# Optimization experiments

Hardware: AMD Instinct MI355X
Metric: run time of the kernel (lower is better)

The kernel has to match this reference:

```python
import jax, jax.numpy as jnp
import numpy as np

N_NODES = 100000
N_EDGES = 1250000
N_FEAT = 64
HIDDEN = 16
N_CLASSES = 7


def setup_inputs() -> dict:
    key = jax.random.key(0)
    ks = jax.random.split(key, 10)
    x = jax.random.normal(ks[0], (N_NODES, N_FEAT), dtype=jnp.float32)
    edge_index = jax.random.randint(ks[1], (2, N_EDGES), 0, N_NODES, dtype=jnp.int64)
    s = 0.1
    return {
        "x": x,
        "edge_index": edge_index,
        # conv1 MLP: Linear(F,16) ReLU Linear(16,16) ReLU
        "W1": jax.random.normal(ks[2], (N_FEAT, HIDDEN), dtype=jnp.float32) * s,
        "b1": jnp.zeros((HIDDEN,), dtype=jnp.float32),
        "W2": jax.random.normal(ks[3], (HIDDEN, HIDDEN), dtype=jnp.float32) * s,
        "b2": jnp.zeros((HIDDEN,), dtype=jnp.float32),
        # conv2 MLP: Linear(16,16) ReLU Linear(16,C)
        "W3": jax.random.normal(ks[4], (HIDDEN, HIDDEN), dtype=jnp.float32) * s,
        "b3": jnp.zeros((HIDDEN,), dtype=jnp.float32),
        "W4": jax.random.normal(ks[5], (HIDDEN, N_CLASSES), dtype=jnp.float32) * s,
        "b4": jnp.zeros((N_CLASSES,), dtype=jnp.float32),
    }


def _gin_aggregate(h, src, dst):
    # GINConv with default eps=0: (1+eps)*x + sum_{j in N(i)} x_j
    msgs = h[src]  # [E, d] gather
    agg = jax.ops.segment_sum(msgs, dst, num_segments=h.shape[0])  # scatter-add
    return h + agg


def reference(x, edge_index, W1, b1, W2, b2, W3, b3, W4, b4):
    src = edge_index[0]
    dst = edge_index[1]
    # conv1: GIN aggregate + MLP(Linear,ReLU,Linear,ReLU)
    h = _gin_aggregate(x, src, dst)
    h = jax.nn.relu(h @ W1 + b1)
    h = jax.nn.relu(h @ W2 + b2)
    # F.relu after conv1 (idempotent here, kept for faithfulness)
    h = jax.nn.relu(h)
    # conv2: GIN aggregate + MLP(Linear,ReLU,Linear)
    h = _gin_aggregate(h, src, dst)
    h = jax.nn.relu(h @ W3 + b3)
    h = h @ W4 + b4
    return jax.nn.log_softmax(h, axis=1)
```

## Files before the change

kernel.cpp:

```cpp
#include <hip/hip_runtime.h>
#include <math.h>

constexpr int NN = 100000;
constexpr int NE = 1250000;
constexpr int NF = 64;
constexpr int NH = 16;
constexpr int NC = 7;

constexpr int BKT_SHIFT = 7;
constexpr int BKT_NODES = 1 << BKT_SHIFT;
constexpr int NBUCKET = (NN + BKT_NODES - 1) / BKT_NODES;
constexpr int BSTRIDE = 2048;
constexpr int EPB = 8192;
constexpr int NBLK_BUCKET = (NE + EPB - 1) / EPB;
constexpr int CUR_PAD = 16;

__global__ __launch_bounds__(256) void k1_gemm(
    const float* __restrict__ x, const float* __restrict__ W1,
    const float* __restrict__ b1, float* __restrict__ A, float* __restrict__ B,
    int* __restrict__ gcur) {
    int gtid = blockIdx.x * 256 + threadIdx.x;
    if (gtid < NBUCKET * CUR_PAD) gcur[gtid] = 0;

    __shared__ float w[NF * NH];
    __shared__ float bias[NH];
    for (int i = threadIdx.x; i < NF * NH; i += blockDim.x) w[i] = W1[i];
    if (threadIdx.x < NH) bias[threadIdx.x] = b1[threadIdx.x];
    __syncthreads();
    int node = gtid;
    if (node >= NN) return;

    float acc[NH];
#pragma unroll
    for (int j = 0; j < NH; ++j) acc[j] = 0.f;

    const float4* xr = (const float4*)(x + (size_t)node * NF);
#pragma unroll
    for (int k4 = 0; k4 < NF / 4; ++k4) {
        float4 xv = xr[k4];
        int k = k4 * 4;
#pragma unroll
        for (int j = 0; j < NH; ++j) {
            acc[j] += xv.x * w[(k + 0) * NH + j]
                    + xv.y * w[(k + 1) * NH + j]
                    + xv.z * w[(k + 2) * NH + j]
                    + xv.w * w[(k + 3) * NH + j];
        }
    }
    float4* Ar = (float4*)(A + (size_t)node * NH);
    float4* Br = (float4*)(B + (size_t)node * NH);
#pragma unroll
    for (int q = 0; q < NH / 4; ++q) {
        float4 a;
        a.x = acc[q * 4 + 0]; a.y = acc[q * 4 + 1];
        a.z = acc[q * 4 + 2]; a.w = acc[q * 4 + 3];
        Ar[q] = a;
        float4 bv;
        bv.x = a.x + bias[q * 4 + 0]; bv.y = a.y + bias[q * 4 + 1];
        bv.z = a.z + bias[q * 4 + 2]; bv.w = a.w + bias[q * 4 + 3];
        Br[q] = bv;
    }
}

__global__ __launch_bounds__(1024) void k_bucket(
    const int* __restrict__ src, const int* __restrict__ dst,
    int* __restrict__ gcur, unsigned* __restrict__ gbuf) {
    __shared__ int cnt[NBUCKET];
    __shared__ int loff[NBUCKET];
    __shared__ int gb[NBUCKET];
    __shared__ int s[1024];
    __shared__ unsigned sorted[EPB];

    int tid = threadIdx.x;
    for (int i = tid; i < NBUCKET; i += 1024) cnt[i] = 0;
    __syncthreads();

    unsigned pk[8];
    int bk[8];
    int rk[8];
    int base = blockIdx.x * EPB;
    int nval = NE - base; if (nval > EPB) nval = EPB;
#pragma unroll
    for (int k = 0; k < 8; ++k) {
        int e = base + k * 1024 + tid;
        bk[k] = -1;
        if (e < NE) {
            int sv = src[e];
            int d = dst[e];
            int b = d >> BKT_SHIFT;
            bk[k] = b;
            pk[k] = ((unsigned)sv << BKT_SHIFT) | (unsigned)(d & (BKT_NODES - 1));
            rk[k] = atomicAdd(&cnt[b], 1);
        }
    }
    __syncthreads();

    int v = (tid < NBUCKET) ? cnt[tid] : 0;
    s[tid] = v;
    __syncthreads();
    for (int d = 1; d < 1024; d <<= 1) {
        int u = (tid >= d) ? s[tid - d] : 0;
        __syncthreads();
        s[tid] += u;
        __syncthreads();
    }
    if (tid < NBUCKET) {
        loff[tid] = s[tid] - v;
        gb[tid] = (v > 0) ? atomicAdd(&gcur[tid * CUR_PAD], v) : 0;
    }
    __syncthreads();

#pragma unroll
    for (int k = 0; k < 8; ++k) {
        if (bk[k] >= 0) sorted[loff[bk[k]] + rk[k]] = pk[k];
    }
    __syncthreads();

    for (int i = tid; i < nval; i += 1024) {
        int lo = 0, hi = NBUCKET - 1;
        while (lo < hi) {
            int mid = (lo + hi + 1) >> 1;
            if (loff[mid] <= i) lo = mid; else hi = mid - 1;
        }
        int pos = gb[lo] + (i - loff[lo]);
        if (pos < BSTRIDE)
            gbuf[(size_t)lo * BSTRIDE + pos] = sorted[i];
    }
}

__global__ __launch_bounds__(512) void k_agg1(
    const float* __restrict__ A, float* __restrict__ B, float* __restrict__ A2,
    const int* __restrict__ gcur, const unsigned* __restrict__ gbuf,
    const float* __restrict__ W2, const float* __restrict__ b2,
    const float* __restrict__ W3, const float* __restrict__ b3) {
    __shared__ unsigned stage[BSTRIDE];
    __shared__ unsigned eSrc[BSTRIDE];
    __shared__ int cnt[BKT_NODES], off[BKT_NODES], cur[BKT_NODES];
    __shared__ float Bl[BKT_NODES * 17];
    __shared__ float Tl[BKT_NODES * 17];
    __shared__ float w2[NH * NH], w3[NH * NH], bb2[NH], bb3[NH];

    int b = blockIdx.x;
    int tid = threadIdx.x;
    for (int i = tid; i < NH * NH; i += 512) { w2[i] = W2[i]; w3[i] = W3[i]; }
    if (tid < NH) { bb2[tid] = b2[tid]; bb3[tid] = b3[tid]; }
    int n = gcur[b * CUR_PAD];
    if (n > BSTRIDE) n = BSTRIDE;
    if (tid < BKT_NODES) cnt[tid] = 0;
    __syncthreads();

    for (int i = tid; i < n; i += 512) {
        unsigned u = gbuf[(size_t)b * BSTRIDE + i];
        stage[i] = u;
        atomicAdd(&cnt[u & (BKT_NODES - 1)], 1);
    }
    __syncthreads();
    if (tid < BKT_NODES) off[tid] = cnt[tid];
    __syncthreads();
    for (int d = 1; d < BKT_NODES; d <<= 1) {
        int v = 0;
        if (tid < BKT_NODES && tid >= d) v = off[tid - d];
        __syncthreads();
        if (tid < BKT_NODES) off[tid] += v;
        __syncthreads();
    }
    if (tid < BKT_NODES) cur[tid] = off[tid] - cnt[tid];
    __syncthreads();
    for (int i = tid; i < n; i += 512) {
        unsigned u = stage[i];
        int pos = atomicAdd(&cur[u & (BKT_NODES - 1)], 1);
        eSrc[pos] = u >> BKT_SHIFT;
    }
    __syncthreads();

    int node = tid >> 2;
    int q = (tid & 3) * 4;
    int gnode = (b << BKT_SHIFT) + node;
    int end = off[node];
    int start = end - cnt[node];

    float4 bq = {0.f, 0.f, 0.f, 0.f};
    if (gnode < NN) bq = *(const float4*)(B + (size_t)gnode * NH + q);
    float4 a0 = {0.f, 0.f, 0.f, 0.f}, a1 = {0.f, 0.f, 0.f, 0.f};
    int j = start;
    for (; j + 2 <= end; j += 2) {
        int s0 = eSrc[j];
        int s1 = eSrc[j + 1];
        float4 v0 = *(const float4*)(A + (size_t)s0 * NH + q);
        float4 v1 = *(const float4*)(A + (size_t)s1 * NH + q);
        a0.x += v0.x; a0.y += v0.y; a0.z += v0.z; a0.w += v0.w;
        a1.x += v1.x; a1.y += v1.y; a1.z += v1.z; a1.w += v1.w;
    }
    if (j < end) {
        int s0 = eSrc[j];
        float4 v0 = *(const float4*)(A + (size_t)s0 * NH + q);
        a0.x += v0.x; a0.y += v0.y; a0.z += v0.z; a0.w += v0.w;
    }
    Bl[node * 17 + q + 0] = fmaxf(bq.x + a0.x + a1.x, 0.f);
    Bl[node * 17 + q + 1] = fmaxf(bq.y + a0.y + a1.y, 0.f);
    Bl[node * 17 + q + 2] = fmaxf(bq.z + a0.z + a1.z, 0.f);
    Bl[node * 17 + q + 3] = fmaxf(bq.w + a0.w + a1.w, 0.f);
    __syncthreads();

    float t0 = bb2[q], t1 = bb2[q + 1], t2 = bb2[q + 2], t3 = bb2[q + 3];
#pragma unroll
    for (int k = 0; k < NH; ++k) {
        float hk = Bl[node * 17 + k];
        t0 += hk * w2[k * NH + q + 0];
        t1 += hk * w2[k * NH + q + 1];
        t2 += hk * w2[k * NH + q + 2];
        t3 += hk * w2[k * NH + q + 3];
    }
    Tl[node * 17 + q + 0] = fmaxf(t0, 0.f);
    Tl[node * 17 + q + 1] = fmaxf(t1, 0.f);
    Tl[node * 17 + q + 2] = fmaxf(t2, 0.f);
    Tl[node * 17 + q + 3] = fmaxf(t3, 0.f);
    __syncthreads();

    float z0 = 0.f, z1 = 0.f, z2 = 0.f, z3 = 0.f;
#pragma unroll
    for (int k = 0; k < NH; ++k) {
        float tk = Tl[node * 17 + k];
        z0 += tk * w3[k * NH + q + 0];
        z1 += tk * w3[k * NH + q + 1];
        z2 += tk * w3[k * NH + q + 2];
        z3 += tk * w3[k * NH + q + 3];
    }
    if (gnode < NN) {
        float4 az = {z0, z1, z2, z3};
        *(float4*)(A2 + (size_t)gnode * NH + q) = az;
        float4 bz = {z0 + bb3[q], z1 + bb3[q + 1], z2 + bb3[q + 2], z3 + bb3[q + 3]};
        *(float4*)(B + (size_t)gnode * NH + q) = bz;
    }
}

__global__ __launch_bounds__(512) void k_agg2(
    const float* __restrict__ A2, const float* __restrict__ B,
    const int* __restrict__ gcur, const unsigned* __restrict__ gbuf,
    const float* __restrict__ W4, const float* __restrict__ b4,
    float* __restrict__ out) {
    __shared__ unsigned stage[BSTRIDE];
    __shared__ unsigned eSrc[BSTRIDE];
    __shared__ int cnt[BKT_NODES], off[BKT_NODES], cur[BKT_NODES];
    __shared__ float Bl[BKT_NODES * 17];
    __shared__ float w4[NH * NC];
    __shared__ float bb4[NC];

    int b = blockIdx.x;
    int tid = threadIdx.x;
    for (int i = tid; i < NH * NC; i += 512) w4[i] = W4[i];
    if (tid < NC) bb4[tid] = b4[tid];
    int n = gcur[b * CUR_PAD];
    if (n > BSTRIDE) n = BSTRIDE;
    if (tid < BKT_NODES) cnt[tid] = 0;
    __syncthreads();

    for (int i = tid; i < n; i += 512) {
        unsigned u = gbuf[(size_t)b * BSTRIDE + i];
        stage[i] = u;
        atomicAdd(&cnt[u & (BKT_NODES - 1)], 1);
    }
    __syncthreads();
    if (tid < BKT_NODES) off[tid] = cnt[tid];
    __syncthreads();
    for (int d = 1; d < BKT_NODES; d <<= 1) {
        int v = 0;
        if (tid < BKT_NODES && tid >= d) v = off[tid - d];
        __syncthreads();
        if (tid < BKT_NODES) off[tid] += v;
        __syncthreads();
    }
    if (tid < BKT_NODES) cur[tid] = off[tid] - cnt[tid];
    __syncthreads();
    for (int i = tid; i < n; i += 512) {
        unsigned u = stage[i];
        int pos = atomicAdd(&cur[u & (BKT_NODES - 1)], 1);
        eSrc[pos] = u >> BKT_SHIFT;
    }
    __syncthreads();

    int node = tid >> 2;
    int q = (tid & 3) * 4;
    int gnode = (b << BKT_SHIFT) + node;
    int end = off[node];
    int start = end - cnt[node];

    float4 bq = {0.f, 0.f, 0.f, 0.f};
    if (gnode < NN) bq = *(const float4*)(B + (size_t)gnode * NH + q);
    float4 a0 = {0.f, 0.f, 0.f, 0.f}, a1 = {0.f, 0.f, 0.f, 0.f};
    int j = start;
    for (; j + 2 <= end; j += 2) {
        int s0 = eSrc[j];
        int s1 = eSrc[j + 1];
        float4 v0 = *(const float4*)(A2 + (size_t)s0 * NH + q);
        float4 v1 = *(const float4*)(A2 + (size_t)s1 * NH + q);
        a0.x += v0.x; a0.y += v0.y; a0.z += v0.z; a0.w += v0.w;
        a1.x += v1.x; a1.y += v1.y; a1.z += v1.z; a1.w += v1.w;
    }
    if (j < end) {
        int s0 = eSrc[j];
        float4 v0 = *(const float4*)(A2 + (size_t)s0 * NH + q);
        a0.x += v0.x; a0.y += v0.y; a0.z += v0.z; a0.w += v0.w;
    }
    Bl[node * 17 + q + 0] = fmaxf(bq.x + a0.x + a1.x, 0.f);
    Bl[node * 17 + q + 1] = fmaxf(bq.y + a0.y + a1.y, 0.f);
    Bl[node * 17 + q + 2] = fmaxf(bq.z + a0.z + a1.z, 0.f);
    Bl[node * 17 + q + 3] = fmaxf(bq.w + a0.w + a1.w, 0.f);
    __syncthreads();

    if (tid < BKT_NODES) {
        int nd = tid;
        int gn = (b << BKT_SHIFT) + nd;
        if (gn < NN) {
            float o[NC];
#pragma unroll
            for (int c = 0; c < NC; ++c) o[c] = bb4[c];
#pragma unroll
            for (int k = 0; k < NH; ++k) {
                float hk = Bl[nd * 17 + k];
#pragma unroll
                for (int c = 0; c < NC; ++c) o[c] += hk * w4[k * NC + c];
            }
            float m = o[0];
#pragma unroll
            for (int c = 1; c < NC; ++c) m = fmaxf(m, o[c]);
            float s = 0.f;
#pragma unroll
            for (int c = 0; c < NC; ++c) s += expf(o[c] - m);
            float ls = m + logf(s);
            float* op = out + (size_t)gn * NC;
#pragma unroll
            for (int c = 0; c < NC; ++c) op[c] = o[c] - ls;
        }
    }
}

extern "C" void kernel_launch(void* const* d_in, const int* in_sizes, int n_in,
                              void* d_out, int out_size, void* d_ws, size_t ws_size,
                              hipStream_t stream) {
    const float* x  = (const float*)d_in[0];
    const int*   ei = (const int*)d_in[1];
    const float* W1 = (const float*)d_in[2];
    const float* b1 = (const float*)d_in[3];
    const float* W2 = (const float*)d_in[4];
    const float* b2 = (const float*)d_in[5];
    const float* W3 = (const float*)d_in[6];
    const float* b3 = (const float*)d_in[7];
    const float* W4 = (const float*)d_in[8];
    const float* b4 = (const float*)d_in[9];
    float* out = (float*)d_out;

    const int* src = ei;
    const int* dst = ei + NE;

    float*    A    = (float*)d_ws;
    float*    B    = A + (size_t)NN * NH;
    float*    A2   = B + (size_t)NN * NH;
    int*      gcur = (int*)(A2 + (size_t)NN * NH);
    unsigned* gbuf = (unsigned*)(gcur + NBUCKET * CUR_PAD);

    const int nodeBlocks = (NN + 255) / 256;

    k1_gemm<<<nodeBlocks, 256, 0, stream>>>(x, W1, b1, A, B, gcur);
    k_bucket<<<NBLK_BUCKET, 1024, 0, stream>>>(src, dst, gcur, gbuf);
    k_agg1<<<NBUCKET, 512, 0, stream>>>(A, B, A2, gcur, gbuf, W2, b2, W3, b3);
    k_agg2<<<NBUCKET, 512, 0, stream>>>(A2, B, gcur, gbuf, W4, b4, out);
}
```

Measured before the change: 81.54 us.

## Reuse per-node sorted edge lists from agg1 in agg2 and drop bucket binary search

k_agg1 now writes its per-node sorted source list back to gbuf, along with per-node offsets and counts as 16-bit arrays. k_agg2 loads these directly instead of redoing the shared-memory count, scan and scatter. k_bucket stores each edge's bucket id in shared memory, which replaces the per-element binary search over loff. It also halves edges per block, giving more blocks and fewer registers per thread, at the cost of more global atomics on the bucket cursors and extra workspace writes.

New measurement: 82.59 us. Within noise of the previous version (+1.3%).

```diff
diff --git a/kernel.cpp b/kernel.cpp
--- a/kernel.cpp
+++ b/kernel.cpp
@@ -11,7 +11,7 @@
 constexpr int BKT_NODES = 1 << BKT_SHIFT;
 constexpr int NBUCKET = (NN + BKT_NODES - 1) / BKT_NODES;
 constexpr int BSTRIDE = 2048;
-constexpr int EPB = 8192;
+constexpr int EPB = 4096;
 constexpr int NBLK_BUCKET = (NE + EPB - 1) / EPB;
 constexpr int CUR_PAD = 16;
 
@@ -70,18 +70,19 @@
     __shared__ int gb[NBUCKET];
     __shared__ int s[1024];
     __shared__ unsigned sorted[EPB];
+    __shared__ unsigned short sortedB[EPB];
 
     int tid = threadIdx.x;
     for (int i = tid; i < NBUCKET; i += 1024) cnt[i] = 0;
     __syncthreads();
 
-    unsigned pk[8];
-    int bk[8];
-    int rk[8];
+    unsigned pk[4];
+    int bk[4];
+    int rk[4];
     int base = blockIdx.x * EPB;
     int nval = NE - base; if (nval > EPB) nval = EPB;
 #pragma unroll
-    for (int k = 0; k < 8; ++k) {
+    for (int k = 0; k < 4; ++k) {
         int e = base + k * 1024 + tid;
         bk[k] = -1;
         if (e < NE) {
@@ -111,26 +112,27 @@
     __syncthreads();
 
 #pragma unroll
-    for (int k = 0; k < 8; ++k) {
-        if (bk[k] >= 0) sorted[loff[bk[k]] + rk[k]] = pk[k];
+    for (int k = 0; k < 4; ++k) {
+        if (bk[k] >= 0) {
+            int p = loff[bk[k]] + rk[k];
+            sorted[p] = pk[k];
+            sortedB[p] = (unsigned short)bk[k];
+        }
     }
     __syncthreads();
 
     for (int i = tid; i < nval; i += 1024) {
-        int lo = 0, hi = NBUCKET - 1;
-        while (lo < hi) {
-            int mid = (lo + hi + 1) >> 1;
-            if (loff[mid] <= i) lo = mid; else hi = mid - 1;
-        }
-        int pos = gb[lo] + (i - loff[lo]);
+        int b = sortedB[i];
+        int pos = gb[b] + (i - loff[b]);
         if (pos < BSTRIDE)
-            gbuf[(size_t)lo * BSTRIDE + pos] = sorted[i];
+            gbuf[(size_t)b * BSTRIDE + pos] = sorted[i];
     }
 }
 
 __global__ __launch_bounds__(512) void k_agg1(
     const float* __restrict__ A, float* __restrict__ B, float* __restrict__ A2,
-    const int* __restrict__ gcur, const unsigned* __restrict__ gbuf,
+    const int* __restrict__ gcur, unsigned* __restrict__ gbuf,
+    unsigned short* __restrict__ soff, unsigned short* __restrict__ scnt,
     const float* __restrict__ W2, const float* __restrict__ b2,
     const float* __restrict__ W3, const float* __restrict__ b3) {
     __shared__ unsigned stage[BSTRIDE];
@@ -164,7 +166,12 @@
         if (tid < BKT_NODES) off[tid] += v;
         __syncthreads();
     }
-    if (tid < BKT_NODES) cur[tid] = off[tid] - cnt[tid];
+    if (tid < BKT_NODES) {
+        int st = off[tid] - cnt[tid];
+        cur[tid] = st;
+        soff[b * BKT_NODES + tid] = (unsigned short)st;
+        scnt[b * BKT_NODES + tid] = (unsigned short)cnt[tid];
+    }
     __syncthreads();
     for (int i = tid; i < n; i += 512) {
         unsigned u = stage[i];
@@ -172,6 +179,8 @@
         eSrc[pos] = u >> BKT_SHIFT;
     }
     __syncthreads();
+
+    for (int i = tid; i < n; i += 512) gbuf[(size_t)b * BSTRIDE + i] = eSrc[i];
 
     int node = tid >> 2;
     int q = (tid & 3) * 4;
@@ -237,11 +246,11 @@
 __global__ __launch_bounds__(512) void k_agg2(
     const float* __restrict__ A2, const float* __restrict__ B,
     const int* __restrict__ gcur, const unsigned* __restrict__ gbuf,
+    const unsigned short* __restrict__ soff, const unsigned short* __restrict__ scnt,
     const float* __restrict__ W4, const float* __restrict__ b4,
     float* __restrict__ out) {
-    __shared__ unsigned stage[BSTRIDE];
     __shared__ unsigned eSrc[BSTRIDE];
-    __shared__ int cnt[BKT_NODES], off[BKT_NODES], cur[BKT_NODES];
+    __shared__ int off[BKT_NODES], cnt[BKT_NODES];
     __shared__ float Bl[BKT_NODES * 17];
     __shared__ float w4[NH * NC];
     __shared__ float bb4[NC];
@@ -252,38 +261,18 @@
     if (tid < NC) bb4[tid] = b4[tid];
     int n = gcur[b * CUR_PAD];
     if (n > BSTRIDE) n = BSTRIDE;
-    if (tid < BKT_NODES) cnt[tid] = 0;
-    __syncthreads();
-
-    for (int i = tid; i < n; i += 512) {
-        unsigned u = gbuf[(size_t)b * BSTRIDE + i];
-        stage[i] = u;
-        atomicAdd(&cnt[u & (BKT_NODES - 1)], 1);
-    }
-    __syncthreads();
-    if (tid < BKT_NODES) off[tid] = cnt[tid];
-    __syncthreads();
-    for (int d = 1; d < BKT_NODES; d <<= 1) {
-        int v = 0;
-        if (tid < BKT_NODES && tid >= d) v = off[tid - d];
-        __syncthreads();
-        if (tid < BKT_NODES) off[tid] += v;
-        __syncthreads();
-    }
-    if (tid < BKT_NODES) cur[tid] = off[tid] - cnt[tid];
-    __syncthreads();
-    for (int i = tid; i < n; i += 512) {
-        unsigned u = stage[i];
-        int pos = atomicAdd(&cur[u & (BKT_NODES - 1)], 1);
-        eSrc[pos] = u >> BKT_SHIFT;
-    }
+    if (tid < BKT_NODES) {
+        off[tid] = soff[b * BKT_NODES + tid];
+        cnt[tid] = scnt[b * BKT_NODES + tid];
+    }
+    for (int i = tid; i < n; i += 512) eSrc[i] = gbuf[(size_t)b * BSTRIDE + i];
     __syncthreads();
 
     int node = tid >> 2;
     int q = (tid & 3) * 4;
     int gnode = (b << BKT_SHIFT) + node;
-    int end = off[node];
-    int start = end - cnt[node];
+    int start = off[node];
+    int end = start + cnt[node];
 
     float4 bq = {0.f, 0.f, 0.f, 0.f};
     if (gnode < NN) bq = *(const float4*)(B + (size_t)gnode * NH + q);
@@ -353,16 +342,18 @@
     const int* src = ei;
     const int* dst = ei + NE;
 
-    float*    A    = (float*)d_ws;
-    float*    B    = A + (size_t)NN * NH;
-    float*    A2   = B + (size_t)NN * NH;
-    int*      gcur = (int*)(A2 + (size_t)NN * NH);
-    unsigned* gbuf = (unsigned*)(gcur + NBUCKET * CUR_PAD);
+    float*          A    = (float*)d_ws;
+    float*          B    = A + (size_t)NN * NH;
+    float*          A2   = B + (size_t)NN * NH;
+    int*            gcur = (int*)(A2 + (size_t)NN * NH);
+    unsigned*       gbuf = (unsigned*)(gcur + NBUCKET * CUR_PAD);
+    unsigned short* soff = (unsigned short*)(gbuf + (size_t)NBUCKET * BSTRIDE);
+    unsigned short* scnt = soff + (size_t)NBUCKET * BKT_NODES;
 
     const int nodeBlocks = (NN + 255) / 256;
 
     k1_gemm<<<nodeBlocks, 256, 0, stream>>>(x, W1, b1, A, B, gcur);
     k_bucket<<<NBLK_BUCKET, 1024, 0, stream>>>(src, dst, gcur, gbuf);
-    k_agg1<<<NBUCKET, 512, 0, stream>>>(A, B, A2, gcur, gbuf, W2, b2, W3, b3);
-    k_agg2<<<NBUCKET, 512, 0, stream>>>(A2, B, gcur, gbuf, W4, b4, out);
-}
+    k_agg1<<<NBUCKET, 512, 0, stream>>>(A, B, A2, gcur, gbuf, soff, scnt, W2, b2, W3, b3);
+    k_agg2<<<NBUCKET, 512, 0, stream>>>(A2, B, gcur, gbuf, soff, scnt, W4, b4, out);
+}
```
